# Kernel tuning notes

Hardware: AMD Instinct MI355X
Metric: run time of the kernel (lower is better)

## Reference

```python
import jax, jax.numpy as jnp
import numpy as np

S, B, D, H, V, TOK = 512, 32, 512, 512, 64, 30000
L = 2  # num LSTM layers


def _lstm_dir(x, Wih, Whh, bih, bhh, reverse):
    # x: [S, B, Din]; Wih: [4H, Din]; Whh: [4H, H]
    Bn = x.shape[1]
    Hn = Whh.shape[1]

    def step(carry, xt):
        h, c = carry
        g = xt @ Wih.T + h @ Whh.T + bih + bhh  # [B, 4H]
        i, f, gg, o = jnp.split(g, 4, axis=-1)  # torch gate order i,f,g,o
        c = jax.nn.sigmoid(f) * c + jax.nn.sigmoid(i) * jnp.tanh(gg)
        h = jax.nn.sigmoid(o) * jnp.tanh(c)
        return (h, c), h

    init = (jnp.zeros((Bn, Hn), x.dtype), jnp.zeros((Bn, Hn), x.dtype))
    _, hs = jax.lax.scan(step, init, x, reverse=reverse)
    return hs  # [S, B, H], time-aligned with x


def _bilstm(x, Wih0, Whh0, bih0, bhh0, Wih1, Whh1, bih1, bhh1):
    # layer 0
    hf = _lstm_dir(x, Wih0[0], Whh0[0], bih0[0], bhh0[0], reverse=False)
    hb = _lstm_dir(x, Wih0[1], Whh0[1], bih0[1], bhh0[1], reverse=True)
    x = jnp.concatenate([hf, hb], axis=-1)  # [S, B, 2H]
    # layer 1
    hf = _lstm_dir(x, Wih1[0], Whh1[0], bih1[0], bhh1[0], reverse=False)
    hb = _lstm_dir(x, Wih1[1], Whh1[1], bih1[1], bhh1[1], reverse=True)
    return jnp.concatenate([hf, hb], axis=-1)  # [S, B, 2H]


def setup_inputs() -> dict:
    key = jax.random.key(0)
    ks = jax.random.split(key, 16)
    s = 0.05
    inp = {}
    inp['source'] = jax.random.randint(ks[0], (S, B), 0, TOK)
    inp['target'] = jax.random.randint(ks[1], (S, B), 0, V)
    inp['emb'] = jax.random.normal(ks[2], (TOK, D), jnp.float32) * s
    inp['Wih0'] = jax.random.normal(ks[3], (2, 4 * H, D), jnp.float32) * s
    inp['Whh0'] = jax.random.normal(ks[4], (2, 4 * H, H), jnp.float32) * s
    inp['bih0'] = jax.random.normal(ks[5], (2, 4 * H), jnp.float32) * s
    inp['bhh0'] = jax.random.normal(ks[6], (2, 4 * H), jnp.float32) * s
    inp['Wih1'] = jax.random.normal(ks[7], (2, 4 * H, 2 * H), jnp.float32) * s
    inp['Whh1'] = jax.random.normal(ks[8], (2, 4 * H, H), jnp.float32) * s
    inp['bih1'] = jax.random.normal(ks[9], (2, 4 * H), jnp.float32) * s
    inp['bhh1'] = jax.random.normal(ks[10], (2, 4 * H), jnp.float32) * s
    inp['Wout'] = jax.random.normal(ks[11], (V, 2 * H), jnp.float32) * s
    inp['bout'] = jax.random.normal(ks[12], (V,), jnp.float32) * s
    inp['trans'] = jax.random.uniform(ks[13], (V, V), jnp.float32)  # torch.rand
    return inp


def reference(source, target, emb, Wih0, Whh0, bih0, bhh0, Wih1, Whh1, bih1, bhh1, Wout, bout, trans):
    # get_logits: frozen embedding -> BiLSTM -> linear
    x = jax.lax.stop_gradient(emb[source])  # [S, B, D] (embedding under no_grad)
    h = _bilstm(x, Wih0, Whh0, bih0, bhh0, Wih1, Whh1, bih1, bhh1)  # [S, B, 2H]
    logits = (h @ Wout.T + bout)[:, 0, :]  # [S, V] -- forward() decodes batch 0

    # Viterbi: max-plus recurrence over time
    def vstep(delta, lt):
        scores = delta[:, None] + trans + lt[None, :]  # [V_prev, V_cur]
        return jnp.max(scores, axis=0), jnp.argmax(scores, axis=0)

    delta, bps = jax.lax.scan(vstep, logits[0], logits[1:])  # bps: [S-1, V]
    last = jnp.argmax(delta)

    def back(idx, bp):
        prev = bp[idx]
        return prev, prev

    _, rev = jax.lax.scan(back, last, bps, reverse=True)  # rev[t] = tag at t, t in [0, S-2]
    path = jnp.concatenate([rev, last[None]]).astype(jnp.int32)  # [S]
    return path
```

## Files before the change

kernel.cpp:

```cpp
#include <hip/hip_runtime.h>
#include <stdint.h>

constexpr int kS = 512;
constexpr int kB = 32;
constexpr int kD = 512;
constexpr int kH = 512;
constexpr int kV = 64;
constexpr int kG = 2048;


__global__ __launch_bounds__(128) void k_embed(const int* __restrict__ src,
                                               const float* __restrict__ emb,
                                               float* __restrict__ X) {
  const int t = blockIdx.x;
  const int s = src[t * kB];
  const float4* e = (const float4*)(emb + (size_t)s * kD);
  float4* x = (float4*)(X + (size_t)t * kD);
  x[threadIdx.x] = e[threadIdx.x];
}

__global__ __launch_bounds__(256) void k_gemm(const float* __restrict__ A0,
                                              const float* __restrict__ A1,
                                              const float* __restrict__ Wih,
                                              const float* __restrict__ bih,
                                              const float* __restrict__ bhh,
                                              float* __restrict__ C, int K) {
  __shared__ float As[16][68];
  __shared__ float Bs[16][68];
  const int d = blockIdx.z;
  const int m0 = blockIdx.y * 64, n0 = blockIdx.x * 64;
  const float* W = Wih + (size_t)d * kG * K;
  const int tid = threadIdx.x;
  const int lr = tid >> 2, lq = tid & 3;
  const int tx = tid & 15, ty = tid >> 4;
  float acc[4][4] = {};
  for (int kb = 0; kb < K; kb += 16) {
    const int k = kb + lq * 4;
    const float* ap = (k < 512) ? (A0 + (size_t)(m0 + lr) * 512 + k)
                                : (A1 + (size_t)(m0 + lr) * 512 + (k - 512));
    const float4 va = *(const float4*)ap;
    const float4 vb = *(const float4*)(W + (size_t)(n0 + lr) * K + k);
    As[lq * 4 + 0][lr] = va.x; As[lq * 4 + 1][lr] = va.y;
    As[lq * 4 + 2][lr] = va.z; As[lq * 4 + 3][lr] = va.w;
    Bs[lq * 4 + 0][lr] = vb.x; Bs[lq * 4 + 1][lr] = vb.y;
    Bs[lq * 4 + 2][lr] = vb.z; Bs[lq * 4 + 3][lr] = vb.w;
    __syncthreads();
#pragma unroll
    for (int kk = 0; kk < 16; kk++) {
      const float4 av = *(const float4*)&As[kk][tx * 4];
      const float4 bv = *(const float4*)&Bs[kk][ty * 4];
      const float a[4] = {av.x, av.y, av.z, av.w};
      const float b[4] = {bv.x, bv.y, bv.z, bv.w};
#pragma unroll
      for (int i = 0; i < 4; i++)
#pragma unroll
        for (int j = 0; j < 4; j++) acc[i][j] += a[i] * b[j];
    }
    __syncthreads();
  }
  float bs[4];
#pragma unroll
  for (int j = 0; j < 4; j++) {
    const int n = n0 + ty * 4 + j;
    bs[j] = bih[d * kG + n] + bhh[d * kG + n];
  }
#pragma unroll
  for (int i = 0; i < 4; i++) {
    const int m = m0 + tx * 4 + i;
    float4 o;
    o.x = acc[i][0] + bs[0]; o.y = acc[i][1] + bs[1];
    o.z = acc[i][2] + bs[2]; o.w = acc[i][3] + bs[3];
    *(float4*)&C[((size_t)d * kS + m) * kG + n0 + ty * 4] = o;
  }
}

__global__ __launch_bounds__(512) void k_rec(const float* __restrict__ Gin,
                                             const float* __restrict__ Whh,
                                             float* __restrict__ Hout) {
  __shared__ float hlds[512];
  __shared__ float part[8 * 128];
  __shared__ float cst[32];
  const int bx = blockIdx.x;
  const int dir = bx & 1, wg = bx >> 1;
  const int tid = threadIdx.x;
  const int wv = tid >> 6, l = tid & 63;
  const float* Wb = Whh + (size_t)dir * kG * kH;
  const float* Gb = Gin + (size_t)dir * kS * kG;
  float* Hb = Hout + (size_t)dir * kS * kH;

  float4 w0[16], w1[16];
  {
    int lr = l;
    int grow = ((lr >> 5) << 9) + wg * 32 + (lr & 31);
    const float4* p = (const float4*)(Wb + (size_t)grow * kH + wv * 64);
#pragma unroll
    for (int i = 0; i < 16; i++) w0[i] = p[i];
    lr = l + 64;
    grow = ((lr >> 5) << 9) + wg * 32 + (lr & 31);
    p = (const float4*)(Wb + (size_t)grow * kH + wv * 64);
#pragma unroll
    for (int i = 0; i < 16; i++) w1[i] = p[i];
  }
  if (tid < 32) cst[tid] = 0.0f;

  for (int s = 0; s < kS; s++) {
    const int t = dir ? (kS - 1 - s) : s;
    float g0 = 0.f, g1 = 0.f, g2 = 0.f, g3 = 0.f;
    if (tid < 32) {
      const float* gp = Gb + (size_t)t * kG + wg * 32 + tid;
      g0 = gp[0]; g1 = gp[512]; g2 = gp[1024]; g3 = gp[1536];
    }
    if (s == 0) {
      hlds[tid] = 0.0f;
    } else {
      const int tp = dir ? (t + 1) : (t - 1);
      unsigned* hp = (unsigned*)(Hb + (size_t)tp * kH);
      unsigned u;
      do {
        u = __hip_atomic_load(hp + tid, __ATOMIC_RELAXED, __HIP_MEMORY_SCOPE_AGENT);
      } while (u == 0xFFFFFFFFu);
      hlds[tid] = __uint_as_float(u);
    }
    __syncthreads();
    float a0x = 0, a0y = 0, a0z = 0, a0w = 0;
    float a1x = 0, a1y = 0, a1z = 0, a1w = 0;
#pragma unroll
    for (int kb = 0; kb < 16; kb++) {
      const float4 hv = *(const float4*)&hlds[wv * 64 + kb * 4];
      a0x += w0[kb].x * hv.x; a0y += w0[kb].y * hv.y;
      a0z += w0[kb].z * hv.z; a0w += w0[kb].w * hv.w;
      a1x += w1[kb].x * hv.x; a1y += w1[kb].y * hv.y;
      a1z += w1[kb].z * hv.z; a1w += w1[kb].w * hv.w;
    }
    part[wv * 128 + l] = (a0x + a0y) + (a0z + a0w);
    part[wv * 128 + 64 + l] = (a1x + a1y) + (a1z + a1w);
    __syncthreads();
    if (tid < 32) {
      float si = g0, sf = g1, sg = g2, so = g3;
#pragma unroll
      for (int w = 0; w < 8; w++) {
        si += part[w * 128 + tid];
        sf += part[w * 128 + 32 + tid];
        sg += part[w * 128 + 64 + tid];
        so += part[w * 128 + 96 + tid];
      }
      float c = cst[tid];
      const float ig = 1.0f / (1.0f + expf(-si));
      const float fg = 1.0f / (1.0f + expf(-sf));
      const float og = 1.0f / (1.0f + expf(-so));
      c = fg * c + ig * tanhf(sg);
      const float h = og * tanhf(c);
      cst[tid] = c;
      __hip_atomic_store((unsigned*)(Hb + (size_t)t * kH) + wg * 32 + tid,
                         __float_as_uint(h), __ATOMIC_RELAXED,
                         __HIP_MEMORY_SCOPE_AGENT);
    }
  }
}

__global__ __launch_bounds__(256) void k_logits(const float* __restrict__ H1,
                                                const float* __restrict__ Wout,
                                                const float* __restrict__ bout,
                                                float* __restrict__ LOG) {
  __shared__ float hl[1024];
  const int t = blockIdx.x;
  const int tid = threadIdx.x;
  float4* hl4 = (float4*)hl;
  if (tid < 128)
    hl4[tid] = ((const float4*)(H1 + (size_t)t * kH))[tid];
  else
    hl4[tid] = ((const float4*)(H1 + (size_t)(kS + t) * kH))[tid - 128];
  __syncthreads();
  const int v = tid >> 2, q = tid & 3;
  const float4* w4 = (const float4*)(Wout + (size_t)v * 1024);
  float4 a = {0, 0, 0, 0};
#pragma unroll 8
  for (int j = 0; j < 64; j++) {
    const int idx = j * 4 + q;
    const float4 w = w4[idx];
    const float4 x = hl4[idx];
    a.x += w.x * x.x; a.y += w.y * x.y; a.z += w.z * x.z; a.w += w.w * x.w;
  }
  float acc = (a.x + a.y) + (a.z + a.w);
  acc += __shfl_xor(acc, 1);
  acc += __shfl_xor(acc, 2);
  if (q == 0) LOG[(size_t)t * kV + v] = acc + bout[v];
}

__global__ __launch_bounds__(256) void k_viterbi(const float* __restrict__ LOG,
                                                 const float* __restrict__ trans,
                                                 int* __restrict__ out) {
  __shared__ float delta[64];
  __shared__ float redS[4 * 64];
  __shared__ int redA[4 * 64];
  __shared__ unsigned char bp[511 * 64];
  const int tid = threadIdx.x;
  const int c = tid & 63, q = tid >> 6;
  if (tid < 64) delta[tid] = LOG[tid];
  __syncthreads();
  for (int t = 1; t < kS; t++) {
    float best = -1e30f;
    int bi = 0;
#pragma unroll 4
    for (int pp = 0; pp < 16; pp++) {
      const int p = q * 16 + pp;
      const float sc = delta[p] + trans[p * 64 + c];
      if (sc > best) { best = sc; bi = p; }
    }
    redS[q * 64 + c] = best;
    redA[q * 64 + c] = bi;
    __syncthreads();
    if (tid < 64) {
      float b = redS[c];
      int a = redA[c];
      for (int qq = 1; qq < 4; qq++) {
        const float v2 = redS[qq * 64 + c];
        if (v2 > b) { b = v2; a = redA[qq * 64 + c]; }
      }
      bp[(t - 1) * 64 + c] = (unsigned char)a;
      delta[c] = b + LOG[t * 64 + c];
    }
    __syncthreads();
  }
  if (tid == 0) {
    float b = delta[0];
    int a = 0;
    for (int i = 1; i < 64; i++)
      if (delta[i] > b) { b = delta[i]; a = i; }
    int idx = a;
    out[kS - 1] = idx;
    for (int t = kS - 2; t >= 0; t--) {
      idx = bp[t * 64 + idx];
      out[t] = idx;
    }
  }
}

extern "C" void kernel_launch(void* const* d_in, const int* in_sizes, int n_in,
                              void* d_out, int out_size, void* d_ws,
                              size_t ws_size, hipStream_t stream) {
  (void)in_sizes; (void)n_in; (void)out_size; (void)ws_size;
  const int* source  = (const int*)d_in[0];
  const float* emb   = (const float*)d_in[2];
  const float* Wih0  = (const float*)d_in[3];
  const float* Whh0  = (const float*)d_in[4];
  const float* bih0  = (const float*)d_in[5];
  const float* bhh0  = (const float*)d_in[6];
  const float* Wih1  = (const float*)d_in[7];
  const float* Whh1  = (const float*)d_in[8];
  const float* bih1  = (const float*)d_in[9];
  const float* bhh1  = (const float*)d_in[10];
  const float* Wout  = (const float*)d_in[11];
  const float* bout  = (const float*)d_in[12];
  const float* trans = (const float*)d_in[13];

  float* ws = (float*)d_ws;
  float* X   = ws;
  float* G0  = ws + 262144;
  float* G1  = ws + 2359296;
  float* H0  = ws + 4456448;
  float* H1  = ws + 4980736;
  float* LOG = ws + 5505024;

  hipMemsetAsync(H0, 0xFF, (size_t)(524288 + 524288) * sizeof(float), stream);

  k_embed<<<kS, 128, 0, stream>>>(source, emb, X);

  dim3 gg(32, 8, 2);
  k_gemm<<<gg, 256, 0, stream>>>(X, X, Wih0, bih0, bhh0, G0, 512);
  k_rec<<<32, 512, 0, stream>>>(G0, Whh0, H0);
  k_gemm<<<gg, 256, 0, stream>>>(H0, H0 + 262144, Wih1, bih1, bhh1, G1, 1024);
  k_rec<<<32, 512, 0, stream>>>(G1, Whh1, H1);
  k_logits<<<kS, 256, 0, stream>>>(H1, Wout, bout, LOG);
  k_viterbi<<<1, 256, 0, stream>>>(LOG, trans, (int*)d_out);
}
```

Measured before the change: 2.335 ms.

## Fuse input projection into recurrent LSTM kernel and widen grid to 64 blocks

```diff
diff --git a/kernel.cpp b/kernel.cpp
--- a/kernel.cpp
+++ b/kernel.cpp
@@ -3,158 +3,136 @@
 
 constexpr int kS = 512;
 constexpr int kB = 32;
-constexpr int kD = 512;
 constexpr int kH = 512;
 constexpr int kV = 64;
-constexpr int kG = 2048;
-
+
+
+__device__ __forceinline__ float fast_sigmoid(float x) {
+  return __builtin_amdgcn_rcpf(1.0f + __expf(-x));
+}
+__device__ __forceinline__ float fast_tanh(float x) {
+  return 1.0f - 2.0f * __builtin_amdgcn_rcpf(1.0f + __expf(2.0f * x));
+}
+__device__ __forceinline__ float bcast(float v, int k) {
+  return __uint_as_float(__builtin_amdgcn_readlane(__float_as_uint(v), k));
+}
 
 __global__ __launch_bounds__(128) void k_embed(const int* __restrict__ src,
                                                const float* __restrict__ emb,
                                                float* __restrict__ X) {
   const int t = blockIdx.x;
   const int s = src[t * kB];
-  const float4* e = (const float4*)(emb + (size_t)s * kD);
-  float4* x = (float4*)(X + (size_t)t * kD);
+  const float4* e = (const float4*)(emb + (size_t)s * 512);
+  float4* x = (float4*)(X + (size_t)t * 512);
   x[threadIdx.x] = e[threadIdx.x];
 }
 
-__global__ __launch_bounds__(256) void k_gemm(const float* __restrict__ A0,
-                                              const float* __restrict__ A1,
-                                              const float* __restrict__ Wih,
-                                              const float* __restrict__ bih,
-                                              const float* __restrict__ bhh,
-                                              float* __restrict__ C, int K) {
-  __shared__ float As[16][68];
-  __shared__ float Bs[16][68];
-  const int d = blockIdx.z;
-  const int m0 = blockIdx.y * 64, n0 = blockIdx.x * 64;
-  const float* W = Wih + (size_t)d * kG * K;
-  const int tid = threadIdx.x;
-  const int lr = tid >> 2, lq = tid & 3;
-  const int tx = tid & 15, ty = tid >> 4;
-  float acc[4][4] = {};
-  for (int kb = 0; kb < K; kb += 16) {
-    const int k = kb + lq * 4;
-    const float* ap = (k < 512) ? (A0 + (size_t)(m0 + lr) * 512 + k)
-                                : (A1 + (size_t)(m0 + lr) * 512 + (k - 512));
-    const float4 va = *(const float4*)ap;
-    const float4 vb = *(const float4*)(W + (size_t)(n0 + lr) * K + k);
-    As[lq * 4 + 0][lr] = va.x; As[lq * 4 + 1][lr] = va.y;
-    As[lq * 4 + 2][lr] = va.z; As[lq * 4 + 3][lr] = va.w;
-    Bs[lq * 4 + 0][lr] = vb.x; Bs[lq * 4 + 1][lr] = vb.y;
-    Bs[lq * 4 + 2][lr] = vb.z; Bs[lq * 4 + 3][lr] = vb.w;
-    __syncthreads();
-#pragma unroll
-    for (int kk = 0; kk < 16; kk++) {
-      const float4 av = *(const float4*)&As[kk][tx * 4];
-      const float4 bv = *(const float4*)&Bs[kk][ty * 4];
-      const float a[4] = {av.x, av.y, av.z, av.w};
-      const float b[4] = {bv.x, bv.y, bv.z, bv.w};
-#pragma unroll
-      for (int i = 0; i < 4; i++)
-#pragma unroll
-        for (int j = 0; j < 4; j++) acc[i][j] += a[i] * b[j];
-    }
-    __syncthreads();
-  }
-  float bs[4];
-#pragma unroll
-  for (int j = 0; j < 4; j++) {
-    const int n = n0 + ty * 4 + j;
-    bs[j] = bih[d * kG + n] + bhh[d * kG + n];
-  }
-#pragma unroll
-  for (int i = 0; i < 4; i++) {
-    const int m = m0 + tx * 4 + i;
-    float4 o;
-    o.x = acc[i][0] + bs[0]; o.y = acc[i][1] + bs[1];
-    o.z = acc[i][2] + bs[2]; o.w = acc[i][3] + bs[3];
-    *(float4*)&C[((size_t)d * kS + m) * kG + n0 + ty * 4] = o;
-  }
-}
-
-__global__ __launch_bounds__(512) void k_rec(const float* __restrict__ Gin,
-                                             const float* __restrict__ Whh,
-                                             float* __restrict__ Hout) {
-  __shared__ float hlds[512];
-  __shared__ float part[8 * 128];
-  __shared__ float cst[32];
+template <int KZ>
+__global__ __launch_bounds__(512, 2) void k_rec(
+    const float* __restrict__ Z0,
+    const float* __restrict__ Z1,
+    const float* __restrict__ Wih,
+    const float* __restrict__ Whh,
+    const float* __restrict__ bih,
+    const float* __restrict__ bhh,
+    float* __restrict__ Hout) {
+  constexpr int ZPW = KZ / 8;
+  __shared__ float part[64 * 9];
+  __shared__ float gsum[64];
   const int bx = blockIdx.x;
   const int dir = bx & 1, wg = bx >> 1;
   const int tid = threadIdx.x;
   const int wv = tid >> 6, l = tid & 63;
-  const float* Wb = Whh + (size_t)dir * kG * kH;
-  const float* Gb = Gin + (size_t)dir * kS * kG;
+  const float* WihB = Wih + (size_t)dir * 2048 * KZ;
+  const float* WhhB = Whh + (size_t)dir * 2048 * 512;
   float* Hb = Hout + (size_t)dir * kS * kH;
-
-  float4 w0[16], w1[16];
+  const int grow = (l >> 4) * 512 + wg * 16 + (l & 15);
+
+  float ww[64];
   {
-    int lr = l;
-    int grow = ((lr >> 5) << 9) + wg * 32 + (lr & 31);
-    const float4* p = (const float4*)(Wb + (size_t)grow * kH + wv * 64);
-#pragma unroll
-    for (int i = 0; i < 16; i++) w0[i] = p[i];
-    lr = l + 64;
-    grow = ((lr >> 5) << 9) + wg * 32 + (lr & 31);
-    p = (const float4*)(Wb + (size_t)grow * kH + wv * 64);
-#pragma unroll
-    for (int i = 0; i < 16; i++) w1[i] = p[i];
-  }
-  if (tid < 32) cst[tid] = 0.0f;
+    const float* wp = WhhB + (size_t)grow * 512 + wv * 64;
+#pragma unroll
+    for (int i = 0; i < 64; i += 4) {
+      const float4 v = *(const float4*)(wp + i);
+      ww[i] = v.x; ww[i + 1] = v.y; ww[i + 2] = v.z; ww[i + 3] = v.w;
+    }
+  }
+  float zw[ZPW];
+  {
+    const float* zp = WihB + (size_t)grow * KZ + wv * ZPW;
+#pragma unroll
+    for (int i = 0; i < ZPW; i += 4) {
+      const float4 v = *(const float4*)(zp + i);
+      zw[i] = v.x; zw[i + 1] = v.y; zw[i + 2] = v.z; zw[i + 3] = v.w;
+    }
+  }
+  float bias = 0.0f;
+  if (tid < 64) {
+    const int gr = (tid >> 4) * 512 + wg * 16 + (tid & 15);
+    bias = bih[dir * 2048 + gr] + bhh[dir * 2048 + gr];
+  }
+  float cstate = 0.0f;
+
+  const float* zbase = (KZ == 512) ? Z0 : ((wv < 4) ? Z0 : Z1);
+  const int zoff = (KZ == 512) ? tid : ((wv & 3) * 128 + l);
+
+  int t0 = dir ? (kS - 1) : 0;
+  float zc0 = zbase[(size_t)t0 * 512 + zoff];
+  float zc1 = (KZ == 1024) ? zbase[(size_t)t0 * 512 + zoff + 64] : 0.0f;
 
   for (int s = 0; s < kS; s++) {
     const int t = dir ? (kS - 1 - s) : s;
-    float g0 = 0.f, g1 = 0.f, g2 = 0.f, g3 = 0.f;
-    if (tid < 32) {
-      const float* gp = Gb + (size_t)t * kG + wg * 32 + tid;
-      g0 = gp[0]; g1 = gp[512]; g2 = gp[1024]; g3 = gp[1536];
-    }
-    if (s == 0) {
-      hlds[tid] = 0.0f;
-    } else {
+    int tn = dir ? (t - 1) : (t + 1);
+    if (tn < 0) tn = 0;
+    if (tn > kS - 1) tn = kS - 1;
+    const float zn0 = zbase[(size_t)tn * 512 + zoff];
+    const float zn1 = (KZ == 1024) ? zbase[(size_t)tn * 512 + zoff + 64] : 0.0f;
+
+    float acc = 0.0f;
+#pragma unroll
+    for (int k = 0; k < 64; k++) acc += zw[k] * bcast(zc0, k);
+    if (KZ == 1024) {
+#pragma unroll
+      for (int k = 0; k < 64; k++) acc += zw[64 + k] * bcast(zc1, k);
+    }
+
+    float hreg = 0.0f;
+    if (s > 0) {
       const int tp = dir ? (t + 1) : (t - 1);
-      unsigned* hp = (unsigned*)(Hb + (size_t)tp * kH);
+      const unsigned* hp = (const unsigned*)(Hb + (size_t)tp * kH) + tid;
       unsigned u;
       do {
-        u = __hip_atomic_load(hp + tid, __ATOMIC_RELAXED, __HIP_MEMORY_SCOPE_AGENT);
+        u = __hip_atomic_load(hp, __ATOMIC_RELAXED, __HIP_MEMORY_SCOPE_AGENT);
       } while (u == 0xFFFFFFFFu);
-      hlds[tid] = __uint_as_float(u);
-    }
-    __syncthreads();
-    float a0x = 0, a0y = 0, a0z = 0, a0w = 0;
-    float a1x = 0, a1y = 0, a1z = 0, a1w = 0;
-#pragma unroll
-    for (int kb = 0; kb < 16; kb++) {
-      const float4 hv = *(const float4*)&hlds[wv * 64 + kb * 4];
-      a0x += w0[kb].x * hv.x; a0y += w0[kb].y * hv.y;
-      a0z += w0[kb].z * hv.z; a0w += w0[kb].w * hv.w;
-      a1x += w1[kb].x * hv.x; a1y += w1[kb].y * hv.y;
-      a1z += w1[kb].z * hv.z; a1w += w1[kb].w * hv.w;
-    }
-    part[wv * 128 + l] = (a0x + a0y) + (a0z + a0w);
-    part[wv * 128 + 64 + l] = (a1x + a1y) + (a1z + a1w);
-    __syncthreads();
-    if (tid < 32) {
-      float si = g0, sf = g1, sg = g2, so = g3;
-#pragma unroll
-      for (int w = 0; w < 8; w++) {
-        si += part[w * 128 + tid];
-        sf += part[w * 128 + 32 + tid];
-        sg += part[w * 128 + 64 + tid];
-        so += part[w * 128 + 96 + tid];
-      }
-      float c = cst[tid];
-      const float ig = 1.0f / (1.0f + expf(-si));
-      const float fg = 1.0f / (1.0f + expf(-sf));
-      const float og = 1.0f / (1.0f + expf(-so));
-      c = fg * c + ig * tanhf(sg);
-      const float h = og * tanhf(c);
-      cst[tid] = c;
-      __hip_atomic_store((unsigned*)(Hb + (size_t)t * kH) + wg * 32 + tid,
+      hreg = __uint_as_float(u);
+    }
+
+#pragma unroll
+    for (int k = 0; k < 64; k++) acc += ww[k] * bcast(hreg, k);
+
+    part[l * 9 + wv] = acc;
+    __syncthreads();
+    if (tid < 64) {
+      float ssum = bias;
+#pragma unroll
+      for (int w = 0; w < 8; w++) ssum += part[tid * 9 + w];
+      gsum[tid] = ssum;
+    }
+    __syncthreads();
+    if (tid < 16) {
+      const float gi = gsum[tid], gf = gsum[16 + tid];
+      const float gg = gsum[32 + tid], go = gsum[48 + tid];
+      const float ig = fast_sigmoid(gi);
+      const float fg = fast_sigmoid(gf);
+      const float og = fast_sigmoid(go);
+      cstate = fg * cstate + ig * fast_tanh(gg);
+      const float h = og * fast_tanh(cstate);
+      __hip_atomic_store((unsigned*)(Hb + (size_t)t * kH) + wg * 16 + tid,
                          __float_as_uint(h), __ATOMIC_RELAXED,
                          __HIP_MEMORY_SCOPE_AGENT);
     }
+    zc0 = zn0;
+    zc1 = zn1;
   }
 }
 
@@ -256,21 +234,15 @@
 
   float* ws = (float*)d_ws;
   float* X   = ws;
-  float* G0  = ws + 262144;
-  float* G1  = ws + 2359296;
-  float* H0  = ws + 4456448;
-  float* H1  = ws + 4980736;
-  float* LOG = ws + 5505024;
-
-  hipMemsetAsync(H0, 0xFF, (size_t)(524288 + 524288) * sizeof(float), stream);
+  float* H0  = ws + 262144;
+  float* H1  = ws + 786432;
+  float* LOG = ws + 1310720;
+
+  hipMemsetAsync(H0, 0xFF, (size_t)1048576 * sizeof(float), stream);
 
   k_embed<<<kS, 128, 0, stream>>>(source, emb, X);
-
-  dim3 gg(32, 8, 2);
-  k_gemm<<<gg, 256, 0, stream>>>(X, X, Wih0, bih0, bhh0, G0, 512);
-  k_rec<<<32, 512, 0, stream>>>(G0, Whh0, H0);
-  k_gemm<<<gg, 256, 0, stream>>>(H0, H0 + 262144, Wih1, bih1, bhh1, G1, 1024);
-  k_rec<<<32, 512, 0, stream>>>(G1, Whh1, H1);
+  k_rec<512><<<64, 512, 0, stream>>>(X, X, Wih0, Whh0, bih0, bhh0, H0);
+  k_rec<1024><<<64, 512, 0, stream>>>(H0, H0 + 262144, Wih1, Whh1, bih1, bhh1, H1);
   k_logits<<<kS, 256, 0, stream>>>(H1, Wout, bout, LOG);
   k_viterbi<<<1, 256, 0, stream>>>(LOG, trans, (int*)d_out);
 }
```

Measured after the change: 2.509 ms. 7.4% more time.
